# Kernel optimization log

Measured on AMD Instinct MI355X. Metric: run time of the kernel, lower is better.

## Reference

```python
import jax, jax.numpy as jnp
import numpy as np

N_IN = 200000
N_OUT = 600000
K = 27          # 3x3x3 kernel offsets
P = 150000      # kernel-map pairs per offset
C_IN = 96
C_OUT = 96
BN_EPS = 1e-5


def setup_inputs() -> dict:
    key = jax.random.key(0)
    k1, k2, k3, k4 = jax.random.split(key, 4)
    feats = jax.random.normal(k1, (N_IN, C_IN), dtype=jnp.float32)
    # kernel map: per offset, input-site indices and output-site indices
    in_idx = jax.random.randint(k2, (K, P), 0, N_IN, dtype=jnp.int32)
    out_idx = jax.random.randint(k3, (K, P), 0, N_OUT, dtype=jnp.int32)
    weight = jax.random.normal(k4, (K, C_IN, C_OUT), dtype=jnp.float32) * (1.0 / np.sqrt(C_IN * K))
    gamma = jnp.ones((C_OUT,), dtype=jnp.float32)
    beta = jnp.zeros((C_OUT,), dtype=jnp.float32)
    return {"feats": feats, "in_idx": in_idx, "out_idx": out_idx,
            "weight": weight, "gamma": gamma, "beta": beta}


def reference(feats, in_idx, out_idx, weight, gamma, beta):
    # Sparse transposed conv: gather -> matmul -> scatter-add per kernel offset.
    out = jnp.zeros((N_OUT, C_OUT), dtype=feats.dtype)
    for k in range(K):  # fixed small loop over kernel offsets (structurally distinct weights)
        contrib = feats[in_idx[k]] @ weight[k]          # [P, C_OUT]
        out = out.at[out_idx[k]].add(contrib)
    # BatchNorm (training-mode batch stats over active output sites), per channel
    mean = jnp.mean(out, axis=0)
    var = jnp.mean((out - mean) ** 2, axis=0)
    y = (out - mean) * jax.lax.rsqrt(var + BN_EPS) * gamma + beta
    # ReLU
    return jax.nn.relu(y)
```

## Files before the change

### kernel.cpp

```cpp
#include <hip/hip_runtime.h>
#include <hip/hip_bf16.h>

#define N_IN   200000
#define N_OUT  600000
#define KOFF   27
#define PPAIR  150000
#define NPAIR  (KOFF * PPAIR)
#define C      96
#define BN_EPS 1e-5f

using bf16x8 = __attribute__((ext_vector_type(8))) __bf16;
using f32x4  = __attribute__((ext_vector_type(4))) float;
using u32x2  = __attribute__((ext_vector_type(2))) unsigned int;
using u32x4  = __attribute__((ext_vector_type(4))) unsigned int;

static __device__ __forceinline__ unsigned short f2b(float x) {
    __hip_bfloat16 h = __float2bfloat16(x);
    return *reinterpret_cast<unsigned short*>(&h);
}
static __device__ __forceinline__ float b_lo(unsigned int u) { return __uint_as_float(u << 16); }
static __device__ __forceinline__ float b_hi(unsigned int u) { return __uint_as_float(u & 0xffff0000u); }

__global__ void cvt_feats(const float* __restrict__ src, unsigned short* __restrict__ dst) {
    int t = blockIdx.x * 256 + threadIdx.x;
    const float4* s4 = (const float4*)src;
    float4 a = s4[2 * t], b = s4[2 * t + 1];
    union { unsigned short u[8]; uint4 v; } r;
    r.u[0] = f2b(a.x); r.u[1] = f2b(a.y); r.u[2] = f2b(a.z); r.u[3] = f2b(a.w);
    r.u[4] = f2b(b.x); r.u[5] = f2b(b.y); r.u[6] = f2b(b.z); r.u[7] = f2b(b.w);
    ((uint4*)dst)[t] = r.v;
}

__global__ void cvt_w(const float* __restrict__ w, unsigned short* __restrict__ wt) {
    int t = blockIdx.x * 256 + threadIdx.x;
    int k = t / 9216;
    int rem = t - k * 9216;
    int o = rem / 96;
    int i = rem - o * 96;
    wt[t] = f2b(w[k * 9216 + i * 96 + o]);
}

__global__ void k_hist(const int* __restrict__ out_idx, int* __restrict__ counts,
                       unsigned char* __restrict__ lrank) {
    int t = blockIdx.x * 256 + threadIdx.x;
    if (t < NPAIR) lrank[t] = (unsigned char)atomicAdd(&counts[out_idx[t]], 1);
}

__global__ void k_bsum(const int* __restrict__ counts, int* __restrict__ bsum) {
    __shared__ int ls[256];
    int b = blockIdx.x, t = threadIdx.x;
    int base = b * 1024 + t * 4;
    int s = 0;
#pragma unroll
    for (int j = 0; j < 4; j++) { int i = base + j; if (i < N_OUT) s += counts[i]; }
    ls[t] = s;
    __syncthreads();
    for (int off = 128; off > 0; off >>= 1) {
        if (t < off) ls[t] += ls[t + off];
        __syncthreads();
    }
    if (t == 0) bsum[b] = ls[0];
}

__global__ void k_scan_bsum(const int* __restrict__ bsum, int* __restrict__ bsum_ex) {
    __shared__ int sc[1024];
    int t = threadIdx.x;
    int v = (t < 586) ? bsum[t] : 0;
    sc[t] = v;
    __syncthreads();
    for (int off = 1; off < 1024; off <<= 1) {
        int add = (t >= off) ? sc[t - off] : 0;
        __syncthreads();
        sc[t] += add;
        __syncthreads();
    }
    bsum_ex[t] = sc[t] - v;
}

__global__ void k_scan_local(int* __restrict__ csr, const int* __restrict__ bsum_ex) {
    __shared__ int sc[256];
    int b = blockIdx.x, t = threadIdx.x;
    int base = b * 1024 + t * 4;
    int c[4];
    int s = 0;
#pragma unroll
    for (int j = 0; j < 4; j++) {
        int i = base + j;
        c[j] = (i < N_OUT) ? csr[i] : 0;
        s += c[j];
    }
    sc[t] = s;
    __syncthreads();
    for (int off = 1; off < 256; off <<= 1) {
        int add = (t >= off) ? sc[t - off] : 0;
        __syncthreads();
        sc[t] += add;
        __syncthreads();
    }
    int run = bsum_ex[b] + sc[t] - s;
#pragma unroll
    for (int j = 0; j < 4; j++) {
        int i = base + j;
        if (i < N_OUT) {
            csr[i] = run;
            run += c[j];
            if (i == N_OUT - 1) csr[N_OUT] = run;
        }
    }
}

__global__ void k_perm(const int* __restrict__ out_idx, const unsigned char* __restrict__ lrank,
                       const int* __restrict__ csr, int* __restrict__ perm) {
    int t = blockIdx.x * 256 + threadIdx.x;
    if (t < NPAIR) perm[csr[out_idx[t]] + (int)lrank[t]] = t;
}

__global__ __launch_bounds__(256, 8) void contrib_k(
    const unsigned short* __restrict__ fb,
    const unsigned short* __restrict__ wt,
    const int* __restrict__ in_idx,
    unsigned short* __restrict__ contrib)
{
    __shared__ __align__(16) unsigned int lds[4][768];

    const int t    = threadIdx.x;
    const int k    = blockIdx.y;
    const int row0 = blockIdx.x * 64;
    const long kp  = (long)k * PPAIR;

    const int wave = t >> 6, lane = t & 63;
    const int quad = lane >> 4, l16 = lane & 15;

    const int pb = row0 + wave * 16 + l16;
    const int pc = (pb < PPAIR) ? pb : (PPAIR - 1);
    const int g  = in_idx[kp + pc];

    const unsigned short* arow  = fb + (size_t)g * 96 + quad * 8;
    const unsigned short* bbase = wt + (size_t)k * 9216 + l16 * 96 + quad * 8;

    f32x4 acc[6];
#pragma unroll
    for (int n = 0; n < 6; n++) acc[n] = (f32x4){0.f, 0.f, 0.f, 0.f};

#pragma unroll
    for (int kk = 0; kk < 3; kk++) {
        bf16x8 a = *(const bf16x8*)(arow + kk * 32);
#pragma unroll
        for (int n = 0; n < 6; n++) {
            bf16x8 b = *(const bf16x8*)(bbase + n * 16 * 96 + kk * 32);
            acc[n] = __builtin_amdgcn_mfma_f32_16x16x32_bf16(b, a, acc[n], 0, 0, 0);
        }
    }

#pragma unroll
    for (int n = 0; n < 6; n++) {
        u32x2 v;
        v.x = (unsigned)f2b(acc[n][0]) | ((unsigned)f2b(acc[n][1]) << 16);
        v.y = (unsigned)f2b(acc[n][2]) | ((unsigned)f2b(acc[n][3]) << 16);
        *(u32x2*)&lds[wave][l16 * 48 + n * 8 + quad * 2] = v;
    }
    __syncthreads();

    const int tile_row0 = row0 + wave * 16;
    if (tile_row0 + 16 <= PPAIR) {
        u32x4* cbase = (u32x4*)contrib;
        const size_t tb = (size_t)(kp + tile_row0) * 12;
#pragma unroll
        for (int s = 0; s < 3; s++) {
            u32x4 v = *(u32x4*)&lds[wave][s * 256 + lane * 4];
            __builtin_nontemporal_store(v, cbase + tb + s * 64 + lane);
        }
    }
}

#define RB_CHUNK 128
__global__ __launch_bounds__(384) void reduce_bn(
    const unsigned short* __restrict__ contrib,
    const int* __restrict__ csr,
    const int* __restrict__ perm,
    float* __restrict__ out,
    float* __restrict__ sums)
{
    __shared__ __align__(16) unsigned short stage[RB_CHUNK * 96];
    __shared__ int   lperm[RB_CHUNK];
    __shared__ int   lcsr[17];
    __shared__ float lsum[96], lq[96];

    const int t  = threadIdx.x;
    const int rl = t / 24, c4 = t - rl * 24;

    float ps0 = 0.f, ps1 = 0.f, ps2 = 0.f, ps3 = 0.f;
    float pq0 = 0.f, pq1 = 0.f, pq2 = 0.f, pq3 = 0.f;

    for (int grp = blockIdx.x; grp < N_OUT / 16; grp += gridDim.x) {
        const int rb = grp * 16;
        if (t < 17) lcsr[t] = csr[rb + t];
        __syncthreads();
        const int s0 = lcsr[0], s1 = lcsr[16];
        const int rs = lcsr[rl], re = lcsr[rl + 1];

        float a0 = 0.f, a1 = 0.f, a2 = 0.f, a3 = 0.f;

        for (int cs = s0; cs < s1; cs += RB_CHUNK) {
            const int ce  = (cs + RB_CHUNK < s1) ? cs + RB_CHUNK : s1;
            const int n12 = (ce - cs) * 12;

            if (t < RB_CHUNK) lperm[t] = (cs + t < s1) ? perm[cs + t] : 0;
            __syncthreads();

            const int i0 = t, i1 = t + 384, i2 = t + 768, i3 = t + 1152;
            const bool g0 = i0 < n12, g1 = i1 < n12, g2 = i2 < n12, g3 = i3 < n12;
            u32x4 v0, v1, v2, v3;
            if (g0) { int e = i0 / 12, s = i0 - (i0 / 12) * 12;
                      v0 = *(const u32x4*)(contrib + (size_t)lperm[e] * 96 + s * 8); }
            if (g1) { int e = i1 / 12, s = i1 - (i1 / 12) * 12;
                      v1 = *(const u32x4*)(contrib + (size_t)lperm[e] * 96 + s * 8); }
            if (g2) { int e = i2 / 12, s = i2 - (i2 / 12) * 12;
                      v2 = *(const u32x4*)(contrib + (size_t)lperm[e] * 96 + s * 8); }
            if (g3) { int e = i3 / 12, s = i3 - (i3 / 12) * 12;
                      v3 = *(const u32x4*)(contrib + (size_t)lperm[e] * 96 + s * 8); }
            if (g0) *(u32x4*)&stage[i0 * 8] = v0;
            if (g1) *(u32x4*)&stage[i1 * 8] = v1;
            if (g2) *(u32x4*)&stage[i2 * 8] = v2;
            if (g3) *(u32x4*)&stage[i3 * 8] = v3;
            __syncthreads();

            const int jb = (rs > cs) ? rs : cs;
            const int je = (re < ce) ? re : ce;
            for (int j = jb; j < je; j++) {
                const unsigned short* sp = stage + (size_t)(j - cs) * 96 + c4 * 4;
                uint2 u = *(const uint2*)sp;
                a0 += b_lo(u.x); a1 += b_hi(u.x); a2 += b_lo(u.y); a3 += b_hi(u.y);
            }
        }

        *(float4*)(out + (size_t)(rb + rl) * 96 + c4 * 4) = make_float4(a0, a1, a2, a3);
        ps0 += a0; ps1 += a1; ps2 += a2; ps3 += a3;
        pq0 += a0 * a0; pq1 += a1 * a1; pq2 += a2 * a2; pq3 += a3 * a3;
        __syncthreads();
    }

    if (t < 96) { lsum[t] = 0.f; lq[t] = 0.f; }
    __syncthreads();
    atomicAdd(&lsum[c4 * 4 + 0], ps0); atomicAdd(&lsum[c4 * 4 + 1], ps1);
    atomicAdd(&lsum[c4 * 4 + 2], ps2); atomicAdd(&lsum[c4 * 4 + 3], ps3);
    atomicAdd(&lq[c4 * 4 + 0], pq0);   atomicAdd(&lq[c4 * 4 + 1], pq1);
    atomicAdd(&lq[c4 * 4 + 2], pq2);   atomicAdd(&lq[c4 * 4 + 3], pq3);
    __syncthreads();
    if (t < 96) {
        atomicAdd(&sums[t], lsum[t]);
        atomicAdd(&sums[96 + t], lq[t]);
    }
}

__global__ void bn_final(float* __restrict__ sums, const float* __restrict__ gamma,
                         const float* __restrict__ beta) {
    int c = threadIdx.x;
    if (c < 96) {
        float mean = sums[c] * (1.0f / (float)N_OUT);
        float var  = sums[96 + c] * (1.0f / (float)N_OUT) - mean * mean;
        float inv  = rsqrtf(var + BN_EPS);
        float sc   = inv * gamma[c];
        sums[c]      = sc;
        sums[96 + c] = beta[c] - mean * sc;
    }
}

__global__ void bn_apply(float* __restrict__ out, const float* __restrict__ sums) {
    int t = blockIdx.x * 256 + threadIdx.x;
    int g = t % 24;
    float sc0 = sums[g * 4 + 0], sc1 = sums[g * 4 + 1];
    float sc2 = sums[g * 4 + 2], sc3 = sums[g * 4 + 3];
    float sh0 = sums[96 + g * 4 + 0], sh1 = sums[96 + g * 4 + 1];
    float sh2 = sums[96 + g * 4 + 2], sh3 = sums[96 + g * 4 + 3];
    f32x4* o4 = (f32x4*)out;
    for (long f = t; f < 14400000L; f += 258048) {
        f32x4 v = __builtin_nontemporal_load(o4 + f);
        v.x = fmaxf(v.x * sc0 + sh0, 0.f);
        v.y = fmaxf(v.y * sc1 + sh1, 0.f);
        v.z = fmaxf(v.z * sc2 + sh2, 0.f);
        v.w = fmaxf(v.w * sc3 + sh3, 0.f);
        __builtin_nontemporal_store(v, o4 + f);
    }
}

extern "C" void kernel_launch(void* const* d_in, const int* in_sizes, int n_in,
                              void* d_out, int out_size, void* d_ws, size_t ws_size,
                              hipStream_t stream) {
    const float* feats  = (const float*)d_in[0];
    const int* in_idx   = (const int*)d_in[1];
    const int* out_idx  = (const int*)d_in[2];
    const float* weight = (const float*)d_in[3];
    const float* gamma  = (const float*)d_in[4];
    const float* beta   = (const float*)d_in[5];
    float* out = (float*)d_out;

    char* ws = (char*)d_ws;
    size_t off = 0;
    unsigned short* fb      = (unsigned short*)(ws + off); off += 38400000;
    unsigned short* wt      = (unsigned short*)(ws + off); off += 497664;
    unsigned short* contrib = (unsigned short*)(ws + off); off += (size_t)NPAIR * 96 * 2;
    int* csr                = (int*)(ws + off); off += 2400016;
    int* bsum               = (int*)(ws + off); off += 4096;
    int* bsum_ex            = (int*)(ws + off); off += 4096;
    unsigned char* lrank    = (unsigned char*)(ws + off); off += NPAIR;
    int* perm               = (int*)(ws + off); off += (size_t)NPAIR * 4;
    float* sums             = (float*)(ws + off); off += 768;

    hipMemsetAsync(csr, 0, (size_t)N_OUT * sizeof(int), stream);
    hipMemsetAsync(sums, 0, 192 * sizeof(float), stream);

    cvt_feats<<<9375, 256, 0, stream>>>(feats, fb);
    cvt_w<<<972, 256, 0, stream>>>(weight, wt);

    k_hist<<<(NPAIR + 255) / 256, 256, 0, stream>>>(out_idx, csr, lrank);
    k_bsum<<<586, 256, 0, stream>>>(csr, bsum);
    k_scan_bsum<<<1, 1024, 0, stream>>>(bsum, bsum_ex);
    k_scan_local<<<586, 256, 0, stream>>>(csr, bsum_ex);
    k_perm<<<(NPAIR + 255) / 256, 256, 0, stream>>>(out_idx, lrank, csr, perm);

    contrib_k<<<dim3(2344, KOFF), 256, 0, stream>>>(fb, wt, in_idx, contrib);

    reduce_bn<<<2500, 384, 0, stream>>>(contrib, csr, perm, out, sums);
    bn_final<<<1, 128, 0, stream>>>(sums, gamma, beta);
    bn_apply<<<1008, 256, 0, stream>>>(out, sums);
}
```

Baseline: 1.308 ms.

## Bin pairs by input-row bucket per offset to localize feature gathers in cache

Adds a histogram, scan and binning pass that groups each offset's pairs into 16 buckets of input rows, with each bucket padded to 64-row tiles. A new contrib kernel walks these bins and interleaves blocks by bucket so that concurrently running blocks gather from a narrow input range, aiming to keep feature rows resident in cache. The perm array now points to padded slots. The LDS staging is also XOR-swizzled to reduce bank conflicts. The cost is several extra passes over the index arrays and a larger contrib buffer, and the path runs only when the workspace is big enough.

```diff
diff --git a/kernel.cpp b/kernel.cpp
--- a/kernel.cpp
+++ b/kernel.cpp
@@ -8,6 +8,11 @@
 #define NPAIR  (KOFF * PPAIR)
 #define C      96
 #define BN_EPS 1e-5f
+
+#define NBUCK  16
+#define BUCKW  12500
+#define NBIN   (KOFF * NBUCK)
+#define PADSLOTS 4077216
 
 using bf16x8 = __attribute__((ext_vector_type(8))) __bf16;
 using f32x4  = __attribute__((ext_vector_type(4))) float;
@@ -115,6 +120,95 @@
     if (t < NPAIR) perm[csr[out_idx[t]] + (int)lrank[t]] = t;
 }
 
+__global__ void k_hist2(const int* __restrict__ in_idx, int* __restrict__ bincnt) {
+    __shared__ int h[NBIN];
+    int t = threadIdx.x;
+    for (int i = t; i < NBIN; i += 256) h[i] = 0;
+    __syncthreads();
+    int gt = blockIdx.x * 256 + t;
+    if (gt < NPAIR) {
+        int k = gt / PPAIR;
+        atomicAdd(&h[k * NBUCK + in_idx[gt] / BUCKW], 1);
+    }
+    __syncthreads();
+    for (int i = t; i < NBIN; i += 256) if (h[i]) atomicAdd(&bincnt[i], h[i]);
+}
+
+__global__ void k_scan2(const int* __restrict__ bincnt, int* __restrict__ pstart,
+                        int* __restrict__ gcursor, int* __restrict__ xpfx) {
+    if (threadIdx.x != 0 || blockIdx.x != 0) return;
+    int acc = 0;
+    for (int b = 0; b < NBIN; b++) {
+        pstart[b] = acc;
+        gcursor[b] = acc;
+        acc += ((bincnt[b] + 63) >> 6) << 6;
+    }
+    pstart[NBIN] = acc;
+    for (int x = 0; x < 8; x++) {
+        int a = 0;
+        for (int i = 0; i < 54; i++) {
+            int bl = x + 8 * (i / 27);
+            int k  = i % 27;
+            xpfx[x * 55 + i] = a;
+            a += (bincnt[k * NBUCK + bl] + 63) >> 6;
+        }
+        xpfx[x * 55 + 54] = a;
+    }
+}
+
+__global__ void k_bin(const int* __restrict__ in_idx, const int* __restrict__ out_idx,
+                      const unsigned char* __restrict__ lrank, const int* __restrict__ csr,
+                      int* __restrict__ gcursor, unsigned short* __restrict__ sg16,
+                      int* __restrict__ perm) {
+    __shared__ int h[NBIN];
+    __shared__ int base[NBIN];
+    int t = threadIdx.x;
+    for (int i = t; i < NBIN; i += 256) h[i] = 0;
+    __syncthreads();
+    int gt = blockIdx.x * 256 + t;
+    int gbin = -1, myloc = 0, g = 0;
+    if (gt < NPAIR) {
+        g = in_idx[gt];
+        gbin = (gt / PPAIR) * NBUCK + g / BUCKW;
+        myloc = atomicAdd(&h[gbin], 1);
+    }
+    __syncthreads();
+    for (int i = t; i < NBIN; i += 256) if (h[i]) base[i] = atomicAdd(&gcursor[i], h[i]);
+    __syncthreads();
+    if (gbin >= 0) {
+        int slot = base[gbin] + myloc;
+        sg16[slot] = (unsigned short)(g - (g / BUCKW) * BUCKW);
+        perm[csr[out_idx[gt]] + (int)lrank[gt]] = slot;
+    }
+}
+
+static __device__ __forceinline__ void tile_store(
+    unsigned int (*lds)[768], int wave, int lane, int quad, int l16,
+    const f32x4* acc, unsigned short* __restrict__ contrib, size_t tile_row0, bool valid)
+{
+    const int swz_w = ((l16 >> 1) & 3) << 2;
+#pragma unroll
+    for (int n = 0; n < 6; n++) {
+        u32x2 v;
+        v.x = (unsigned)f2b(acc[n][0]) | ((unsigned)f2b(acc[n][1]) << 16);
+        v.y = (unsigned)f2b(acc[n][2]) | ((unsigned)f2b(acc[n][3]) << 16);
+        *(u32x2*)&lds[wave][l16 * 48 + ((n * 8 + quad * 2) ^ swz_w)] = v;
+    }
+    __syncthreads();
+    if (valid) {
+        u32x4* cbase = (u32x4*)contrib;
+        const size_t tb = tile_row0 * 12;
+#pragma unroll
+        for (int s = 0; s < 3; s++) {
+            const int w   = s * 256 + lane * 4;
+            const int row = w / 48;
+            const int o   = w - row * 48;
+            u32x4 v = *(u32x4*)&lds[wave][row * 48 + (o ^ (((row >> 1) & 3) << 2))];
+            __builtin_nontemporal_store(v, cbase + tb + s * 64 + lane);
+        }
+    }
+}
+
 __global__ __launch_bounds__(256, 8) void contrib_k(
     const unsigned short* __restrict__ fb,
     const unsigned short* __restrict__ wt,
@@ -141,7 +235,6 @@
     f32x4 acc[6];
 #pragma unroll
     for (int n = 0; n < 6; n++) acc[n] = (f32x4){0.f, 0.f, 0.f, 0.f};
-
 #pragma unroll
     for (int kk = 0; kk < 3; kk++) {
         bf16x8 a = *(const bf16x8*)(arow + kk * 32);
@@ -152,25 +245,57 @@
         }
     }
 
-#pragma unroll
-    for (int n = 0; n < 6; n++) {
-        u32x2 v;
-        v.x = (unsigned)f2b(acc[n][0]) | ((unsigned)f2b(acc[n][1]) << 16);
-        v.y = (unsigned)f2b(acc[n][2]) | ((unsigned)f2b(acc[n][3]) << 16);
-        *(u32x2*)&lds[wave][l16 * 48 + n * 8 + quad * 2] = v;
-    }
-    __syncthreads();
-
     const int tile_row0 = row0 + wave * 16;
-    if (tile_row0 + 16 <= PPAIR) {
-        u32x4* cbase = (u32x4*)contrib;
-        const size_t tb = (size_t)(kp + tile_row0) * 12;
-#pragma unroll
-        for (int s = 0; s < 3; s++) {
-            u32x4 v = *(u32x4*)&lds[wave][s * 256 + lane * 4];
-            __builtin_nontemporal_store(v, cbase + tb + s * 64 + lane);
-        }
-    }
+    tile_store(lds, wave, lane, quad, l16, acc, contrib,
+               (size_t)(kp + tile_row0), tile_row0 + 16 <= PPAIR);
+}
+
+__global__ __launch_bounds__(256, 8) void contrib_kb(
+    const unsigned short* __restrict__ fb,
+    const unsigned short* __restrict__ wt,
+    const unsigned short* __restrict__ sg16,
+    const int* __restrict__ pstart,
+    const int* __restrict__ xpfx,
+    unsigned short* __restrict__ contrib)
+{
+    __shared__ __align__(16) unsigned int lds[4][768];
+
+    const int bid = blockIdx.x;
+    const int x = bid & 7, j = bid >> 3;
+    if (j >= xpfx[x * 55 + 54]) return;
+    int i = 0;
+    while (j >= xpfx[x * 55 + i + 1]) i++;
+    const int bl   = x + 8 * (i / 27);
+    const int k    = i % 27;
+    const int jj   = j - xpfx[x * 55 + i];
+    const int slot0 = pstart[k * NBUCK + bl] + jj * 64;
+    const int brow  = bl * BUCKW;
+
+    const int t    = threadIdx.x;
+    const int wave = t >> 6, lane = t & 63;
+    const int quad = lane >> 4, l16 = lane & 15;
+
+    const int slot = slot0 + wave * 16 + l16;
+    const int grow = brow + (int)sg16[slot];
+
+    const unsigned short* arow  = fb + (size_t)grow * 96 + quad * 8;
+    const unsigned short* bbase = wt + (size_t)k * 9216 + l16 * 96 + quad * 8;
+
+    f32x4 acc[6];
+#pragma unroll
+    for (int n = 0; n < 6; n++) acc[n] = (f32x4){0.f, 0.f, 0.f, 0.f};
+#pragma unroll
+    for (int kk = 0; kk < 3; kk++) {
+        bf16x8 a = *(const bf16x8*)(arow + kk * 32);
+#pragma unroll
+        for (int n = 0; n < 6; n++) {
+            bf16x8 b = *(const bf16x8*)(bbase + n * 16 * 96 + kk * 32);
+            acc[n] = __builtin_amdgcn_mfma_f32_16x16x32_bf16(b, a, acc[n], 0, 0, 0);
+        }
+    }
+
+    tile_store(lds, wave, lane, quad, l16, acc, contrib,
+               (size_t)(slot0 + wave * 16), true);
 }
 
 #define RB_CHUNK 128
@@ -295,16 +420,27 @@
     const float* beta   = (const float*)d_in[5];
     float* out = (float*)d_out;
 
+    const size_t NEED = 38400000ULL + 497664 + (size_t)PADSLOTS * 192 + 2400016
+                      + 4096 + 4096 + NPAIR + (size_t)NPAIR * 4 + (size_t)PADSLOTS * 2
+                      + 1728 + 1744 + 1728 + 1760 + 768;
+    const bool big = (ws_size >= NEED);
+
     char* ws = (char*)d_ws;
     size_t off = 0;
     unsigned short* fb      = (unsigned short*)(ws + off); off += 38400000;
     unsigned short* wt      = (unsigned short*)(ws + off); off += 497664;
-    unsigned short* contrib = (unsigned short*)(ws + off); off += (size_t)NPAIR * 96 * 2;
+    unsigned short* contrib = (unsigned short*)(ws + off);
+    off += big ? (size_t)PADSLOTS * 192 : (size_t)NPAIR * 192;
     int* csr                = (int*)(ws + off); off += 2400016;
     int* bsum               = (int*)(ws + off); off += 4096;
     int* bsum_ex            = (int*)(ws + off); off += 4096;
     unsigned char* lrank    = (unsigned char*)(ws + off); off += NPAIR;
     int* perm               = (int*)(ws + off); off += (size_t)NPAIR * 4;
+    unsigned short* sg16    = (unsigned short*)(ws + off); off += big ? (size_t)PADSLOTS * 2 : 0;
+    int* bincnt             = (int*)(ws + off); off += 1728;
+    int* pstart             = (int*)(ws + off); off += 1744;
+    int* gcursor            = (int*)(ws + off); off += 1728;
+    int* xpfx               = (int*)(ws + off); off += 1760;
     float* sums             = (float*)(ws + off); off += 768;
 
     hipMemsetAsync(csr, 0, (size_t)N_OUT * sizeof(int), stream);
@@ -317,9 +453,18 @@
     k_bsum<<<586, 256, 0, stream>>>(csr, bsum);
     k_scan_bsum<<<1, 1024, 0, stream>>>(bsum, bsum_ex);
     k_scan_local<<<586, 256, 0, stream>>>(csr, bsum_ex);
-    k_perm<<<(NPAIR + 255) / 256, 256, 0, stream>>>(out_idx, lrank, csr, perm);
-
-    contrib_k<<<dim3(2344, KOFF), 256, 0, stream>>>(fb, wt, in_idx, contrib);
+
+    if (big) {
+        hipMemsetAsync(bincnt, 0, NBIN * sizeof(int), stream);
+        k_hist2<<<(NPAIR + 255) / 256, 256, 0, stream>>>(in_idx, bincnt);
+        k_scan2<<<1, 64, 0, stream>>>(bincnt, pstart, gcursor, xpfx);
+        k_bin<<<(NPAIR + 255) / 256, 256, 0, stream>>>(in_idx, out_idx, lrank, csr,
+                                                       gcursor, sg16, perm);
+        contrib_kb<<<8 * 8096, 256, 0, stream>>>(fb, wt, sg16, pstart, xpfx, contrib);
+    } else {
+        k_perm<<<(NPAIR + 255) / 256, 256, 0, stream>>>(out_idx, lrank, csr, perm);
+        contrib_k<<<dim3(2344, KOFF), 256, 0, stream>>>(fb, wt, in_idx, contrib);
+    }
 
     reduce_bn<<<2500, 384, 0, stream>>>(contrib, csr, perm, out, sums);
     bn_final<<<1, 128, 0, stream>>>(sums, gamma, beta);
```

New measurement: 1.394 ms. +6.6%, slower.
